# Kernel tuning notes

Hardware: AMD Instinct MI355X
Metric: run time of the kernel (lower is better)

The kernel has to match this reference:

```python
import jax, jax.numpy as jnp
import numpy as np

N_NODES = 100000
N_EDGES = 250000
EMB = 32
NUM_RELS2 = 100   # 2 * num_rels
NUM_TYPES = 16


def _xavier(key, shape):
    fan_in, fan_out = shape[-2], shape[-1]
    limit = float(np.sqrt(6.0 / (fan_in + fan_out)))
    return jax.random.uniform(key, shape, jnp.float32, -limit, limit)


def setup_inputs() -> dict:
    key = jax.random.key(0)
    ks = jax.random.split(key, 9)
    src_ids = jax.random.randint(ks[0], (N_NODES,), 0, N_NODES)
    edge_src = jax.random.randint(ks[1], (N_EDGES,), 0, N_NODES)
    edge_dst = jax.random.randint(ks[2], (N_EDGES,), 0, N_NODES)
    etype = jax.random.randint(ks[3], (N_EDGES,), 0, NUM_RELS2)
    entity = _xavier(ks[4], (N_NODES, EMB))
    W1 = _xavier(ks[5], (NUM_RELS2, EMB, EMB))
    W2 = _xavier(ks[6], (NUM_RELS2, EMB, NUM_TYPES))
    lambda_w = _xavier(ks[7], (NUM_TYPES, 1))
    lambda_b = jnp.zeros((1,), jnp.float32)
    return {
        "entity": entity, "W1": W1, "W2": W2,
        "lambda_w": lambda_w, "lambda_b": lambda_b,
        "src_ids": src_ids, "edge_src": edge_src,
        "edge_dst": edge_dst, "etype": etype,
    }


def _rgcn_layer(h, W, edge_src, edge_dst, etype, n_dst, activation):
    # gather per-edge relation weights [E, in, out] and per-edge bmm (as DGL does)
    msg = jnp.einsum('ed,edo->eo', h[edge_src], W[etype])  # [E, out]
    s = jax.ops.segment_sum(msg, edge_dst, num_segments=n_dst)  # [N, out]
    deg = jax.ops.segment_sum(jnp.ones((msg.shape[0],), msg.dtype),
                              edge_dst, num_segments=n_dst)
    out = s / jnp.maximum(deg, 1.0)[:, None]  # mean; 0 for isolated dst nodes
    if activation is not None:
        out = activation(out)
    return out


def reference(entity, W1, W2, lambda_w, lambda_b,
              src_ids, edge_src, edge_dst, etype):
    # eval mode: dropout disabled; self_loop=False, bias=False
    h = entity[src_ids]                                            # [N, EMB]
    h = _rgcn_layer(h, W1, edge_src, edge_dst, etype, N_NODES, jax.nn.relu)
    h = _rgcn_layer(h, W2, edge_src, edge_dst, etype, N_NODES, None)  # [N, T]
    # PonderNet loop, max_steps=2: step1 lambda from linear+sigmoid, step2 lambda=1
    lam = jax.nn.sigmoid(h @ lambda_w + lambda_b)[:, 0]            # [N]
    p = jnp.stack([lam, 1.0 - lam])                                # [2, N]
    # recomputed h at step 2 is identical (same params, no dropout)
    y = jnp.stack([h, h])                                          # [2, N, T]
    return (y, p)
```

## Files before the change

kernel.cpp:

```cpp
#include <hip/hip_runtime.h>
#include <hip/hip_bf16.h>

#define N_NODES 100000
#define N_EDGES 250000
#define EMB 32
#define TYPES 16
#define R2 100
#define SB 1024
#define NB ((N_EDGES + SB - 1) / SB)
#define NBN ((N_NODES + SB - 1) / SB)
#define S1 64
#define S2 64

typedef __attribute__((ext_vector_type(8))) short short8;
typedef __attribute__((ext_vector_type(4))) float f32x4;

__device__ __forceinline__ unsigned short f2bf_u(float f) {
    unsigned u = __float_as_uint(f);
    u = (u + 0x7fffu + ((u >> 16) & 1u)) >> 16;
    return (unsigned short)u;
}
__device__ __forceinline__ float bfl(unsigned u) { return __uint_as_float(u << 16); }
__device__ __forceinline__ float bfh(unsigned u) { return __uint_as_float(u & 0xffff0000u); }

__global__ __launch_bounds__(SB) void hist_conv_kernel(
        const int* __restrict__ etype, const int* __restrict__ edge_dst,
        const float* __restrict__ entity,
        int* __restrict__ counts, int* __restrict__ dcnt,
        unsigned short* __restrict__ ent_bf) {
    __shared__ int lh[R2];
    int t = threadIdx.x, b = blockIdx.x;
    if (t < R2) lh[t] = 0;
    __syncthreads();
    int e = b * SB + t;
    if (e < N_EDGES) {
        atomicAdd(&lh[etype[e]], 1);
        atomicAdd(&dcnt[edge_dst[e]], 1);
    }
    if (e < 2 * N_NODES) {
        int node = e >> 1, half = e & 1;
        const float4* src = (const float4*)(entity + (size_t)node * EMB + half * 16);
        ushort4* dst = (ushort4*)(ent_bf + (size_t)node * EMB + half * 16);
#pragma unroll
        for (int i = 0; i < 4; ++i) {
            float4 v = src[i];
            ushort4 o = { f2bf_u(v.x), f2bf_u(v.y), f2bf_u(v.z), f2bf_u(v.w) };
            dst[i] = o;
        }
    }
    __syncthreads();
    if (t < R2) counts[b * R2 + t] = lh[t];
}

__global__ __launch_bounds__(SB) void scan_fused_kernel(
        const int* __restrict__ dcnt, int* __restrict__ dstart,
        int* __restrict__ partials,
        const int* __restrict__ counts, int* __restrict__ basem,
        int* __restrict__ total,
        const float* __restrict__ W1, const float* __restrict__ W2,
        unsigned short* __restrict__ pw1, unsigned short* __restrict__ pw2) {
    __shared__ int sd[SB];
    int t = threadIdx.x, b = blockIdx.x;
    if (b < NBN) {
        int i = b * SB + t;
        int v = (i < N_NODES) ? dcnt[i] : 0;
        sd[t] = v;
        __syncthreads();
        for (int o = 1; o < SB; o <<= 1) {
            int x = (t >= o) ? sd[t - o] : 0;
            __syncthreads();
            sd[t] += x;
            __syncthreads();
        }
        if (i < N_NODES) dstart[i] = sd[t] - v;
        if (t == SB - 1) partials[b] = sd[t];
    } else {
        int r = b - NBN;
        int v = (t < NB) ? counts[t * R2 + r] : 0;
        sd[t] = v;
        __syncthreads();
        for (int o = 1; o < SB; o <<= 1) {
            int x = (t >= o) ? sd[t - o] : 0;
            __syncthreads();
            sd[t] += x;
            __syncthreads();
        }
        if (t < NB) basem[t * R2 + r] = sd[t] - v;
        if (t == SB - 1) total[r] = sd[t];

        const float* Wr1 = W1 + (size_t)r * (EMB * EMB);
        {
            int l = t >> 4, j = t & 15;
            int n = l & 15, q = l >> 4;
            int k = q * 8 + (j & 7);
            int col = (j < 8) ? n : (16 + n);
            pw1[(size_t)r * 1024 + t] = f2bf_u(Wr1[k * EMB + col]);
        }
        if (t < 512) {
            const float* Wr2 = W2 + (size_t)r * (EMB * TYPES);
            int l = t >> 3, j = t & 7;
            int n = l & 15, q = l >> 4;
            int k = q * 8 + j;
            pw2[(size_t)r * 512 + t] = f2bf_u(Wr2[k * TYPES + n]);
        }
    }
}

__global__ __launch_bounds__(256) void scanB2_kernel(const int* __restrict__ total,
                                                     int* __restrict__ off,
                                                     int* __restrict__ partials) {
    __shared__ int sd[256];
    int t = threadIdx.x;
    if (blockIdx.x == 0) {
        int v = (t < R2) ? total[t] : 0;
        sd[t] = v;
        __syncthreads();
        for (int o = 1; o < 256; o <<= 1) {
            int x = (t >= o) ? sd[t - o] : 0; __syncthreads();
            sd[t] += x; __syncthreads();
        }
        if (t < R2) off[t] = sd[t] - v;
        if (t == R2 - 1) off[R2] = sd[t];
    } else {
        int v = (t < NBN) ? partials[t] : 0;
        sd[t] = v;
        __syncthreads();
        for (int o = 1; o < 256; o <<= 1) {
            int x = (t >= o) ? sd[t - o] : 0; __syncthreads();
            sd[t] += x; __syncthreads();
        }
        if (t < NBN) partials[t] = sd[t] - v;
    }
}

__global__ __launch_bounds__(SB) void scatter_kernel(
        const int* __restrict__ edge_src, const int* __restrict__ edge_dst,
        const int* __restrict__ etype, const int* __restrict__ src_ids,
        const int* __restrict__ basem, const int* __restrict__ off,
        const int* __restrict__ dstart, const int* __restrict__ partials,
        int* __restrict__ dcur, int4* __restrict__ epack) {
    __shared__ int lh[R2];
    int t = threadIdx.x, b = blockIdx.x;
    if (t < R2) lh[t] = 0;
    __syncthreads();
    int e = b * SB + t;
    if (e >= N_EDGES) return;
    int r = etype[e];
    int rank = atomicAdd(&lh[r], 1);
    int relpos = off[r] + basem[b * R2 + r] + rank;
    int d = edge_dst[e];
    int drank = atomicAdd(&dcur[d], 1);
    int s = edge_src[e];
    int4 v = { src_ids[s], s, dstart[d] + partials[d >> 10] + drank, 0 };
    epack[relpos] = v;
}

__global__ __launch_bounds__(64) void layer1_kernel(
        const unsigned short* __restrict__ ent_bf,
        const unsigned short* __restrict__ pw1,
        const int* __restrict__ off, const int4* __restrict__ epack,
        unsigned short* __restrict__ msg1) {
    int r = blockIdx.x % R2, stripe = blockIdx.x / R2;
    int lo = off[r], hi = off[r + 1];
    int nT = (hi - lo + 15) >> 4;
    int lane = threadIdx.x;
    int n = lane & 15, q = lane >> 4;
    short8 b0 = *(const short8*)(pw1 + (size_t)r * 1024 + lane * 16);
    short8 b1 = *(const short8*)(pw1 + (size_t)r * 1024 + lane * 16 + 8);
    for (int g = stripe; g < nT; g += S1) {
        int base = lo + g * 16;
        int cl = hi - base;
        int me = n < cl ? n : cl - 1;
        int sid = epack[base + me].x;
        short8 a = *(const short8*)(ent_bf + (size_t)sid * EMB + q * 8);
        f32x4 c0 = {0.f,0.f,0.f,0.f}, c1 = {0.f,0.f,0.f,0.f};
        c0 = __builtin_amdgcn_mfma_f32_16x16x32_bf16(a, b0, c0, 0, 0, 0);
        c1 = __builtin_amdgcn_mfma_f32_16x16x32_bf16(a, b1, c1, 0, 0, 0);
#pragma unroll
        for (int i = 0; i < 4; ++i) {
            int row = q * 4 + i;
            if (row < cl) {
                int p = epack[base + row].z;
                msg1[(size_t)p * EMB + n]      = f2bf_u(c0[i]);
                msg1[(size_t)p * EMB + 16 + n] = f2bf_u(c1[i]);
            }
        }
    }
}

__global__ void reduce1_kernel(const unsigned int* __restrict__ msg1,
                               const int* __restrict__ dstart,
                               const int* __restrict__ partials,
                               const int* __restrict__ dcnt,
                               unsigned int* __restrict__ h1bf) {
    int t = blockIdx.x * blockDim.x + threadIdx.x;
    if (t >= N_NODES * 16) return;
    int nn = t >> 4, cp = t & 15;
    int s = dstart[nn] + partials[nn >> 10];
    int cnt = dcnt[nn];
    float sx = 0.f, sy = 0.f;
    for (int k = 0; k < cnt; ++k) {
        unsigned v = msg1[(size_t)(s + k) * 16 + cp];
        sx += bfl(v); sy += bfh(v);
    }
    float inv = 1.0f / fmaxf((float)cnt, 1.0f);
    unsigned lo = f2bf_u(fmaxf(sx * inv, 0.f));
    unsigned hi = f2bf_u(fmaxf(sy * inv, 0.f));
    h1bf[t] = lo | (hi << 16);
}

__global__ __launch_bounds__(64) void layer2_kernel(
        const unsigned short* __restrict__ h1bf,
        const unsigned short* __restrict__ pw2,
        const int* __restrict__ off, const int4* __restrict__ epack,
        unsigned short* __restrict__ msg2) {
    int r = blockIdx.x % R2, stripe = blockIdx.x / R2;
    int lo = off[r], hi = off[r + 1];
    int nT = (hi - lo + 15) >> 4;
    int lane = threadIdx.x;
    int n = lane & 15, q = lane >> 4;
    short8 b = *(const short8*)(pw2 + (size_t)r * 512 + lane * 8);
    for (int g = stripe; g < nT; g += S2) {
        int base = lo + g * 16;
        int cl = hi - base;
        int me = n < cl ? n : cl - 1;
        int s = epack[base + me].y;
        short8 a = *(const short8*)(h1bf + (size_t)s * EMB + q * 8);
        f32x4 c = {0.f,0.f,0.f,0.f};
        c = __builtin_amdgcn_mfma_f32_16x16x32_bf16(a, b, c, 0, 0, 0);
#pragma unroll
        for (int i = 0; i < 4; ++i) {
            int row = q * 4 + i;
            if (row < cl) {
                int p = epack[base + row].z;
                msg2[(size_t)p * TYPES + n] = f2bf_u(c[i]);
            }
        }
    }
}

__global__ void reduce2_head_kernel(const unsigned int* __restrict__ msg2,
                                    const int* __restrict__ dstart,
                                    const int* __restrict__ partials,
                                    const int* __restrict__ dcnt,
                                    const float* __restrict__ lw,
                                    const float* __restrict__ lb,
                                    float* __restrict__ out) {
    int nn = blockIdx.x * blockDim.x + threadIdx.x;
    if (nn >= N_NODES) return;
    int s = dstart[nn] + partials[nn >> 10];
    int cnt = dcnt[nn];

    float h[TYPES];
#pragma unroll
    for (int j = 0; j < TYPES; ++j) h[j] = 0.f;
    for (int k = 0; k < cnt; ++k) {
        const uint4* row = (const uint4*)(msg2 + (size_t)(s + k) * 8);
        uint4 A = row[0], B = row[1];
        h[0] += bfl(A.x);  h[1] += bfh(A.x);  h[2] += bfl(A.y);  h[3] += bfh(A.y);
        h[4] += bfl(A.z);  h[5] += bfh(A.z);  h[6] += bfl(A.w);  h[7] += bfh(A.w);
        h[8] += bfl(B.x);  h[9] += bfh(B.x);  h[10] += bfl(B.y); h[11] += bfh(B.y);
        h[12] += bfl(B.z); h[13] += bfh(B.z); h[14] += bfl(B.w); h[15] += bfh(B.w);
    }
    float inv = 1.0f / fmaxf((float)cnt, 1.0f);
    float dot = 0.f;
#pragma unroll
    for (int j = 0; j < TYPES; ++j) { h[j] *= inv; dot += h[j] * lw[j]; }
    dot += lb[0];
    float lam = 1.0f / (1.0f + expf(-dot));

    float4* y0 = (float4*)(out + (size_t)nn * TYPES);
    float4* y1 = (float4*)(out + (size_t)N_NODES * TYPES + (size_t)nn * TYPES);
#pragma unroll
    for (int j = 0; j < 4; ++j) {
        float4 v = { h[4*j], h[4*j+1], h[4*j+2], h[4*j+3] };
        y0[j] = v; y1[j] = v;
    }
    out[(size_t)2 * N_NODES * TYPES + nn] = lam;
    out[(size_t)2 * N_NODES * TYPES + N_NODES + nn] = 1.0f - lam;
}

extern "C" void kernel_launch(void* const* d_in, const int* in_sizes, int n_in,
                              void* d_out, int out_size, void* d_ws, size_t ws_size,
                              hipStream_t stream) {
    const float* entity = (const float*)d_in[0];
    const float* W1     = (const float*)d_in[1];
    const float* W2     = (const float*)d_in[2];
    const float* lw     = (const float*)d_in[3];
    const float* lb     = (const float*)d_in[4];
    const int* src_ids  = (const int*)d_in[5];
    const int* edge_src = (const int*)d_in[6];
    const int* edge_dst = (const int*)d_in[7];
    const int* etype    = (const int*)d_in[8];
    float* out = (float*)d_out;

    unsigned int* W = (unsigned int*)d_ws;
    int* dcnt      = (int*)(W + 0);
    int* dcur      = (int*)(W + 100000);
    int* dstart    = (int*)(W + 200000);
    int* partials  = (int*)(W + 300008);
    int* counts    = (int*)(W + 300136);
    int* basem     = (int*)(W + 324636);
    int* total     = (int*)(W + 349136);
    int* off       = (int*)(W + 349264);
    int4* epack    = (int4*)(W + 349408);
    unsigned short* ent_bf = (unsigned short*)(W + 1349408);
    unsigned short* pw1    = (unsigned short*)(W + 2949408);
    unsigned short* pw2    = (unsigned short*)(W + 3000608);
    unsigned int* msg1     = (unsigned int*)(W + 3026208);
    unsigned int* h1bf     = (unsigned int*)(W + 7026208);
    unsigned int* msg2     = (unsigned int*)(W + 8626208);

    (void)hipMemsetAsync(d_ws, 0, 200000 * sizeof(int), stream);

    hist_conv_kernel<<<NB, SB, 0, stream>>>(etype, edge_dst, entity,
                                            counts, dcnt, ent_bf);
    scan_fused_kernel<<<NBN + R2, SB, 0, stream>>>(dcnt, dstart, partials,
                                                   counts, basem, total,
                                                   W1, W2, pw1, pw2);
    scanB2_kernel<<<2, 256, 0, stream>>>(total, off, partials);
    scatter_kernel<<<NB, SB, 0, stream>>>(edge_src, edge_dst, etype, src_ids,
                                          basem, off, dstart, partials, dcur, epack);
    layer1_kernel<<<R2 * S1, 64, 0, stream>>>(ent_bf, pw1, off, epack,
                                              (unsigned short*)msg1);
    reduce1_kernel<<<(N_NODES * 16 + 255) / 256, 256, 0, stream>>>(
        msg1, dstart, partials, dcnt, h1bf);
    layer2_kernel<<<R2 * S2, 64, 0, stream>>>((const unsigned short*)h1bf, pw2,
                                              off, epack, (unsigned short*)msg2);
    reduce2_head_kernel<<<(N_NODES + 255) / 256, 256, 0, stream>>>(
        msg2, dstart, partials, dcnt, lw, lb, out);
}
```

Before: 151.7 us.

## Use wave-shuffle scans, fold second-level scan into scatter, split edge pack arrays

The block-wide Hillis-Steele LDS scans, which need many barriers, are replaced with wave shuffle scans plus a small cross-wave step. The separate scanB2 kernel is removed: each scatter block recomputes the relation offsets and partial prefixes itself, and block 0 writes them to global memory. The int4 edge pack becomes three separate int arrays so each layer reads only the fields it needs. Layer1's message writes are packed into one 32-bit store per lane, with the W1 column permutation changed to match. The cost is redundant scan work in every scatter block.

Result: no change. 153.9 us (+1.5%).

```diff
diff --git a/kernel.cpp b/kernel.cpp
--- a/kernel.cpp
+++ b/kernel.cpp
@@ -22,6 +22,15 @@
 }
 __device__ __forceinline__ float bfl(unsigned u) { return __uint_as_float(u << 16); }
 __device__ __forceinline__ float bfh(unsigned u) { return __uint_as_float(u & 0xffff0000u); }
+
+__device__ __forceinline__ int wave_incl_scan(int v, int lane) {
+#pragma unroll
+    for (int o = 1; o < 64; o <<= 1) {
+        int x = __shfl_up(v, o);
+        if (lane >= o) v += x;
+    }
+    return v;
+}
 
 __global__ __launch_bounds__(SB) void hist_conv_kernel(
         const int* __restrict__ etype, const int* __restrict__ edge_dst,
@@ -59,41 +68,56 @@
         int* __restrict__ total,
         const float* __restrict__ W1, const float* __restrict__ W2,
         unsigned short* __restrict__ pw1, unsigned short* __restrict__ pw2) {
-    __shared__ int sd[SB];
+    __shared__ int ws[16];
     int t = threadIdx.x, b = blockIdx.x;
+    int lane = t & 63, w = t >> 6;
     if (b < NBN) {
         int i = b * SB + t;
         int v = (i < N_NODES) ? dcnt[i] : 0;
-        sd[t] = v;
+        int inc = wave_incl_scan(v, lane);
+        if (lane == 63) ws[w] = inc;
         __syncthreads();
-        for (int o = 1; o < SB; o <<= 1) {
-            int x = (t >= o) ? sd[t - o] : 0;
-            __syncthreads();
-            sd[t] += x;
-            __syncthreads();
-        }
-        if (i < N_NODES) dstart[i] = sd[t] - v;
-        if (t == SB - 1) partials[b] = sd[t];
+        if (t < 16) {
+            int s = ws[t];
+            int inc2 = s;
+#pragma unroll
+            for (int o = 1; o < 16; o <<= 1) {
+                int x = __shfl_up(inc2, o);
+                if (t >= o) inc2 += x;
+            }
+            ws[t] = inc2;
+        }
+        __syncthreads();
+        int base = (w == 0) ? 0 : ws[w - 1];
+        if (i < N_NODES) dstart[i] = base + inc - v;
+        if (t == SB - 1) partials[b] = ws[15];
     } else {
         int r = b - NBN;
         int v = (t < NB) ? counts[t * R2 + r] : 0;
-        sd[t] = v;
+        int inc = wave_incl_scan(v, lane);
+        if (lane == 63) ws[w] = inc;
         __syncthreads();
-        for (int o = 1; o < SB; o <<= 1) {
-            int x = (t >= o) ? sd[t - o] : 0;
-            __syncthreads();
-            sd[t] += x;
-            __syncthreads();
-        }
-        if (t < NB) basem[t * R2 + r] = sd[t] - v;
-        if (t == SB - 1) total[r] = sd[t];
+        if (t < 16) {
+            int s = ws[t];
+            int inc2 = s;
+#pragma unroll
+            for (int o = 1; o < 16; o <<= 1) {
+                int x = __shfl_up(inc2, o);
+                if (t >= o) inc2 += x;
+            }
+            ws[t] = inc2;
+        }
+        __syncthreads();
+        int base = (w == 0) ? 0 : ws[w - 1];
+        if (t < NB) basem[t * R2 + r] = base + inc - v;
+        if (t == 0) total[r] = ws[15];
 
         const float* Wr1 = W1 + (size_t)r * (EMB * EMB);
         {
             int l = t >> 4, j = t & 15;
             int n = l & 15, q = l >> 4;
             int k = q * 8 + (j & 7);
-            int col = (j < 8) ? n : (16 + n);
+            int col = 2 * n + (j >> 3);
             pw1[(size_t)r * 1024 + t] = f2bf_u(Wr1[k * EMB + col]);
         }
         if (t < 512) {
@@ -106,62 +130,70 @@
     }
 }
 
-__global__ __launch_bounds__(256) void scanB2_kernel(const int* __restrict__ total,
-                                                     int* __restrict__ off,
-                                                     int* __restrict__ partials) {
-    __shared__ int sd[256];
-    int t = threadIdx.x;
-    if (blockIdx.x == 0) {
-        int v = (t < R2) ? total[t] : 0;
-        sd[t] = v;
-        __syncthreads();
-        for (int o = 1; o < 256; o <<= 1) {
-            int x = (t >= o) ? sd[t - o] : 0; __syncthreads();
-            sd[t] += x; __syncthreads();
-        }
-        if (t < R2) off[t] = sd[t] - v;
-        if (t == R2 - 1) off[R2] = sd[t];
-    } else {
-        int v = (t < NBN) ? partials[t] : 0;
-        sd[t] = v;
-        __syncthreads();
-        for (int o = 1; o < 256; o <<= 1) {
-            int x = (t >= o) ? sd[t - o] : 0; __syncthreads();
-            sd[t] += x; __syncthreads();
-        }
-        if (t < NBN) partials[t] = sd[t] - v;
-    }
-}
-
 __global__ __launch_bounds__(SB) void scatter_kernel(
         const int* __restrict__ edge_src, const int* __restrict__ edge_dst,
         const int* __restrict__ etype, const int* __restrict__ src_ids,
-        const int* __restrict__ basem, const int* __restrict__ off,
-        const int* __restrict__ dstart, const int* __restrict__ partials,
-        int* __restrict__ dcur, int4* __restrict__ epack) {
+        const int* __restrict__ basem, const int* __restrict__ total,
+        const int* __restrict__ partials, const int* __restrict__ dstart,
+        int* __restrict__ dcur,
+        int* __restrict__ sid, int* __restrict__ srcn, int* __restrict__ pdst,
+        int* __restrict__ off_g, int* __restrict__ psg) {
     __shared__ int lh[R2];
+    __shared__ int off_s[R2 + 1];
+    __shared__ int ps_s[NBN];
     int t = threadIdx.x, b = blockIdx.x;
+    int lane = t & 63, w = t >> 6;
     if (t < R2) lh[t] = 0;
+    if (w == 0) {
+        int a = (lane < R2) ? total[lane] : 0;
+        int ai = wave_incl_scan(a, lane);
+        int t0 = __shfl(ai, 63);
+        int i2 = lane + 64;
+        int c = (i2 < R2) ? total[i2] : 0;
+        int ci = wave_incl_scan(c, lane) + t0;
+        off_s[lane] = ai - a;
+        if (i2 < R2) off_s[i2] = ci - c;
+        if (i2 == R2 - 1) off_s[R2] = ci;
+        if (b == 0) {
+            off_g[lane] = ai - a;
+            if (i2 < R2) off_g[i2] = ci - c;
+            if (i2 == R2 - 1) off_g[R2] = ci;
+        }
+    } else if (w == 1) {
+        int a = (lane < NBN) ? partials[lane] : 0;
+        int ai = wave_incl_scan(a, lane);
+        int t0 = __shfl(ai, 63);
+        int i2 = lane + 64;
+        int c = (i2 < NBN) ? partials[i2] : 0;
+        int ci = wave_incl_scan(c, lane) + t0;
+        ps_s[lane] = ai - a;
+        if (i2 < NBN) ps_s[i2] = ci - c;
+        if (b == 0) {
+            psg[lane] = ai - a;
+            if (i2 < NBN) psg[i2] = ci - c;
+        }
+    }
     __syncthreads();
     int e = b * SB + t;
     if (e >= N_EDGES) return;
     int r = etype[e];
     int rank = atomicAdd(&lh[r], 1);
-    int relpos = off[r] + basem[b * R2 + r] + rank;
+    int relpos = off_s[r] + basem[b * R2 + r] + rank;
     int d = edge_dst[e];
     int drank = atomicAdd(&dcur[d], 1);
     int s = edge_src[e];
-    int4 v = { src_ids[s], s, dstart[d] + partials[d >> 10] + drank, 0 };
-    epack[relpos] = v;
+    sid[relpos] = src_ids[s];
+    srcn[relpos] = s;
+    pdst[relpos] = dstart[d] + ps_s[d >> 10] + drank;
 }
 
 __global__ __launch_bounds__(64) void layer1_kernel(
         const unsigned short* __restrict__ ent_bf,
         const unsigned short* __restrict__ pw1,
-        const int* __restrict__ off, const int4* __restrict__ epack,
-        unsigned short* __restrict__ msg1) {
+        const int* __restrict__ off_g, const int* __restrict__ sid,
+        const int* __restrict__ pdst, unsigned int* __restrict__ msg1) {
     int r = blockIdx.x % R2, stripe = blockIdx.x / R2;
-    int lo = off[r], hi = off[r + 1];
+    int lo = off_g[r], hi = off_g[r + 1];
     int nT = (hi - lo + 15) >> 4;
     int lane = threadIdx.x;
     int n = lane & 15, q = lane >> 4;
@@ -171,8 +203,8 @@
         int base = lo + g * 16;
         int cl = hi - base;
         int me = n < cl ? n : cl - 1;
-        int sid = epack[base + me].x;
-        short8 a = *(const short8*)(ent_bf + (size_t)sid * EMB + q * 8);
+        int sv = sid[base + me];
+        short8 a = *(const short8*)(ent_bf + (size_t)sv * EMB + q * 8);
         f32x4 c0 = {0.f,0.f,0.f,0.f}, c1 = {0.f,0.f,0.f,0.f};
         c0 = __builtin_amdgcn_mfma_f32_16x16x32_bf16(a, b0, c0, 0, 0, 0);
         c1 = __builtin_amdgcn_mfma_f32_16x16x32_bf16(a, b1, c1, 0, 0, 0);
@@ -180,9 +212,9 @@
         for (int i = 0; i < 4; ++i) {
             int row = q * 4 + i;
             if (row < cl) {
-                int p = epack[base + row].z;
-                msg1[(size_t)p * EMB + n]      = f2bf_u(c0[i]);
-                msg1[(size_t)p * EMB + 16 + n] = f2bf_u(c1[i]);
+                int p = pdst[base + row];
+                msg1[(size_t)p * 16 + n] =
+                    (unsigned)f2bf_u(c0[i]) | ((unsigned)f2bf_u(c1[i]) << 16);
             }
         }
     }
@@ -190,13 +222,13 @@
 
 __global__ void reduce1_kernel(const unsigned int* __restrict__ msg1,
                                const int* __restrict__ dstart,
-                               const int* __restrict__ partials,
+                               const int* __restrict__ psg,
                                const int* __restrict__ dcnt,
                                unsigned int* __restrict__ h1bf) {
     int t = blockIdx.x * blockDim.x + threadIdx.x;
     if (t >= N_NODES * 16) return;
     int nn = t >> 4, cp = t & 15;
-    int s = dstart[nn] + partials[nn >> 10];
+    int s = dstart[nn] + psg[nn >> 10];
     int cnt = dcnt[nn];
     float sx = 0.f, sy = 0.f;
     for (int k = 0; k < cnt; ++k) {
@@ -212,10 +244,10 @@
 __global__ __launch_bounds__(64) void layer2_kernel(
         const unsigned short* __restrict__ h1bf,
         const unsigned short* __restrict__ pw2,
-        const int* __restrict__ off, const int4* __restrict__ epack,
-        unsigned short* __restrict__ msg2) {
+        const int* __restrict__ off_g, const int* __restrict__ srcn,
+        const int* __restrict__ pdst, unsigned short* __restrict__ msg2) {
     int r = blockIdx.x % R2, stripe = blockIdx.x / R2;
-    int lo = off[r], hi = off[r + 1];
+    int lo = off_g[r], hi = off_g[r + 1];
     int nT = (hi - lo + 15) >> 4;
     int lane = threadIdx.x;
     int n = lane & 15, q = lane >> 4;
@@ -224,7 +256,7 @@
         int base = lo + g * 16;
         int cl = hi - base;
         int me = n < cl ? n : cl - 1;
-        int s = epack[base + me].y;
+        int s = srcn[base + me];
         short8 a = *(const short8*)(h1bf + (size_t)s * EMB + q * 8);
         f32x4 c = {0.f,0.f,0.f,0.f};
         c = __builtin_amdgcn_mfma_f32_16x16x32_bf16(a, b, c, 0, 0, 0);
@@ -232,7 +264,7 @@
         for (int i = 0; i < 4; ++i) {
             int row = q * 4 + i;
             if (row < cl) {
-                int p = epack[base + row].z;
+                int p = pdst[base + row];
                 msg2[(size_t)p * TYPES + n] = f2bf_u(c[i]);
             }
         }
@@ -241,14 +273,14 @@
 
 __global__ void reduce2_head_kernel(const unsigned int* __restrict__ msg2,
                                     const int* __restrict__ dstart,
-                                    const int* __restrict__ partials,
+                                    const int* __restrict__ psg,
                                     const int* __restrict__ dcnt,
                                     const float* __restrict__ lw,
                                     const float* __restrict__ lb,
                                     float* __restrict__ out) {
     int nn = blockIdx.x * blockDim.x + threadIdx.x;
     if (nn >= N_NODES) return;
-    int s = dstart[nn] + partials[nn >> 10];
+    int s = dstart[nn] + psg[nn >> 10];
     int cnt = dcnt[nn];
 
     float h[TYPES];
@@ -302,14 +334,17 @@
     int* counts    = (int*)(W + 300136);
     int* basem     = (int*)(W + 324636);
     int* total     = (int*)(W + 349136);
-    int* off       = (int*)(W + 349264);
-    int4* epack    = (int4*)(W + 349408);
-    unsigned short* ent_bf = (unsigned short*)(W + 1349408);
-    unsigned short* pw1    = (unsigned short*)(W + 2949408);
-    unsigned short* pw2    = (unsigned short*)(W + 3000608);
-    unsigned int* msg1     = (unsigned int*)(W + 3026208);
-    unsigned int* h1bf     = (unsigned int*)(W + 7026208);
-    unsigned int* msg2     = (unsigned int*)(W + 8626208);
+    int* off_g     = (int*)(W + 349264);
+    int* psg       = (int*)(W + 349392);
+    int* sid       = (int*)(W + 349520);
+    int* srcn      = (int*)(W + 599520);
+    int* pdst      = (int*)(W + 849520);
+    unsigned short* ent_bf = (unsigned short*)(W + 1099520);
+    unsigned short* pw1    = (unsigned short*)(W + 2699520);
+    unsigned short* pw2    = (unsigned short*)(W + 2750720);
+    unsigned int* msg1     = (unsigned int*)(W + 2776320);
+    unsigned int* h1bf     = (unsigned int*)(W + 6776320);
+    unsigned int* msg2     = (unsigned int*)(W + 8376320);
 
     (void)hipMemsetAsync(d_ws, 0, 200000 * sizeof(int), stream);
 
@@ -318,15 +353,15 @@
     scan_fused_kernel<<<NBN + R2, SB, 0, stream>>>(dcnt, dstart, partials,
                                                    counts, basem, total,
                                                    W1, W2, pw1, pw2);
-    scanB2_kernel<<<2, 256, 0, stream>>>(total, off, partials);
     scatter_kernel<<<NB, SB, 0, stream>>>(edge_src, edge_dst, etype, src_ids,
-                                          basem, off, dstart, partials, dcur, epack);
-    layer1_kernel<<<R2 * S1, 64, 0, stream>>>(ent_bf, pw1, off, epack,
-                                              (unsigned short*)msg1);
+                                          basem, total, partials, dstart, dcur,
+                                          sid, srcn, pdst, off_g, psg);
+    layer1_kernel<<<R2 * S1, 64, 0, stream>>>(ent_bf, pw1, off_g, sid, pdst, msg1);
     reduce1_kernel<<<(N_NODES * 16 + 255) / 256, 256, 0, stream>>>(
-        msg1, dstart, partials, dcnt, h1bf);
+        msg1, dstart, psg, dcnt, h1bf);
     layer2_kernel<<<R2 * S2, 64, 0, stream>>>((const unsigned short*)h1bf, pw2,
-                                              off, epack, (unsigned short*)msg2);
+                                              off_g, srcn, pdst,
+                                              (unsigned short*)msg2);
     reduce2_head_kernel<<<(N_NODES + 255) / 256, 256, 0, stream>>>(
-        msg2, dstart, partials, dcnt, lw, lb, out);
-}
+        msg2, dstart, psg, dcnt, lw, lb, out);
+}
```
